# Performance work log

Hardware: AMD Instinct MI355X
Metric: run time of the kernel (lower is better)

## Reference

```python
import jax, jax.numpy as jnp
import numpy as np

N_NODES = 50000


def setup_inputs() -> dict:
    key = jax.random.key(0)
    k1, k2, k3, k4, k5, k6 = jax.random.split(key, 6)
    c_in, c_out = 64, 64
    n_edges = 800000
    G = jax.random.normal(k1, (N_NODES, c_in), dtype=jnp.float32)
    RSC = jax.random.normal(k2, (N_NODES, c_in), dtype=jnp.float32)
    src = jax.random.randint(k3, (n_edges,), 0, N_NODES, dtype=jnp.int64)
    dst = jax.random.randint(k4, (n_edges,), 0, N_NODES, dtype=jnp.int64)
    W = jax.random.normal(k5, (c_out, c_in), dtype=jnp.float32) / np.sqrt(c_in)
    b = jax.random.normal(k6, (c_out,), dtype=jnp.float32) * 0.01
    return {"G": G, "RSC": RSC, "src": src, "dst": dst, "W": W, "b": b}


def reference(G, RSC, src, dst, W, b):
    # Per-edge relative feature: src node 'G' feature minus dst node 'RSC' feature
    rel = G[src] - RSC[dst]                          # [E, c_in]
    # Linear + ReLU (edge MLP)
    enc = jax.nn.relu(rel @ W.T + b)                 # [E, c_out]
    # Per-dst-node reductions over variable-size mailboxes
    max_agg = jax.ops.segment_max(enc, dst, num_segments=N_NODES)  # -inf for empty
    sum_agg = jax.ops.segment_sum(enc, dst, num_segments=N_NODES)
    cnt = jax.ops.segment_sum(jnp.ones_like(dst, dtype=enc.dtype), dst,
                              num_segments=N_NODES)               # [N]
    has_mail = (cnt > 0)[:, None]
    avg_agg = sum_agg / jnp.maximum(cnt, 1.0)[:, None]
    max_agg = jnp.where(has_mail, max_agg, 0.0)      # nodes w/o edges -> 0
    # concat(max, avg) as in reduce()
    return jnp.concatenate([max_agg, avg_agg], axis=-1)  # [N, 2*c_out]
```

## Files before the change

kernel.cpp:

```cpp
#include <hip/hip_runtime.h>
#include <hip/hip_bf16.h>

#define NCH 64
#define SPAN 64
#define BIN_BLOCKS 128
#define BIN_THREADS 1024
#define HIST_BLOCKS 256
#define SORT_CAP 3072

__global__ void detect_init_kernel(const unsigned short* __restrict__ gp, int n16,
                                   const unsigned* __restrict__ ip, int niw,
                                   unsigned* __restrict__ flags,
                                   unsigned* __restrict__ gcnt, int nb) {
    if (blockIdx.x == 0) {
        __shared__ unsigned se, so;
        if (threadIdx.x == 0) { se = 0u; so = 0u; }
        __syncthreads();
        unsigned le = 0u, lo = 0u;
        for (int i = threadIdx.x; i < n16; i += blockDim.x) {
            unsigned ex = (unsigned)((gp[i] >> 7) & 0xFFu);
            if (ex >= 0xC0u) le++;
        }
        for (int i = threadIdx.x; i < niw; i += blockDim.x) {
            if ((i & 1) && ip[i] != 0u) lo++;
        }
        atomicAdd(&se, le);
        atomicAdd(&so, lo);
        __syncthreads();
        if (threadIdx.x == 0) {
            flags[0] = (se > 50u) ? 1u : 0u;
            flags[1] = (so < 50u) ? 1u : 0u;
        }
    } else {
        const int stride = (gridDim.x - 1) * blockDim.x;
        for (int i = (blockIdx.x - 1) * blockDim.x + threadIdx.x; i < nb; i += stride)
            gcnt[i] = 0u;
    }
}

__global__ void bucket_hist_kernel(const void* __restrict__ dstp,
                                   unsigned* __restrict__ gcnt,
                                   const unsigned* __restrict__ flags,
                                   int n_edges, int nb) {
    extern __shared__ unsigned lcnt[];
    for (int i = threadIdx.x; i < nb; i += blockDim.x) lcnt[i] = 0u;
    __syncthreads();
    const unsigned i64 = flags[1];
    const int stride = gridDim.x * blockDim.x;
    for (int e = blockIdx.x * blockDim.x + threadIdx.x; e < n_edges; e += stride) {
        int d = i64 ? (int)((const long long*)dstp)[e] : ((const int*)dstp)[e];
        atomicAdd(&lcnt[d >> 6], 1u);
    }
    __syncthreads();
    for (int i = threadIdx.x; i < nb; i += blockDim.x)
        if (lcnt[i]) atomicAdd(&gcnt[i], lcnt[i]);
}

__global__ void bucket_scan_kernel(const unsigned* __restrict__ gcnt,
                                   unsigned* __restrict__ boffs,
                                   unsigned* __restrict__ cursor, int nb) {
    __shared__ unsigned s[1024];
    const int t = threadIdx.x;
    const int L = (nb + 1023) / 1024;
    unsigned local = 0u;
    for (int i = 0; i < L; ++i) {
        int idx = t * L + i;
        if (idx < nb) local += gcnt[idx];
    }
    s[t] = local;
    __syncthreads();
    for (int off = 1; off < 1024; off <<= 1) {
        unsigned v = (t >= off) ? s[t - off] : 0u;
        __syncthreads();
        s[t] += v;
        __syncthreads();
    }
    unsigned run = s[t] - local;
    for (int i = 0; i < L; ++i) {
        int idx = t * L + i;
        if (idx < nb) { boffs[idx] = run; cursor[idx] = run; run += gcnt[idx]; }
    }
}

__global__ __launch_bounds__(BIN_THREADS)
void binning_kernel(const void* __restrict__ srcp, const void* __restrict__ dstp,
                    unsigned* __restrict__ cursor, unsigned* __restrict__ binned,
                    const unsigned* __restrict__ flags, int n_edges, int nb, int depth) {
    extern __shared__ unsigned lds[];
    unsigned* lcnt = lds;
    unsigned* stage = lds + nb;
    for (int i = threadIdx.x; i < nb; i += blockDim.x) lcnt[i] = 0u;
    __syncthreads();
    const unsigned i64 = flags[1];
    const int chunk = (n_edges + gridDim.x - 1) / gridDim.x;
    const int e0 = blockIdx.x * chunk;
    const int e1 = min(e0 + chunk, n_edges);
    for (int e = e0 + threadIdx.x; e < e1; e += blockDim.x) {
        int s, d;
        if (i64) {
            s = (int)((const long long*)srcp)[e];
            d = (int)((const long long*)dstp)[e];
        } else {
            s = ((const int*)srcp)[e];
            d = ((const int*)dstp)[e];
        }
        const int b = d >> 6;
        const unsigned pk = ((unsigned)(d & 63) << 26) | (unsigned)s;
        unsigned pos = atomicAdd(&lcnt[b], 1u);
        if ((int)pos < depth) {
            stage[b * depth + (int)pos] = pk;
        } else {
            unsigned g = atomicAdd(&cursor[b], 1u);
            binned[g] = pk;
        }
    }
    __syncthreads();
    for (int b = threadIdx.x; b < nb; b += blockDim.x) {
        int k = min((int)lcnt[b], depth);
        if (k > 0) {
            unsigned base = atomicAdd(&cursor[b], (unsigned)k);
            for (int i = 0; i < k; ++i) binned[base + i] = stage[b * depth + i];
        }
    }
}

__global__ __launch_bounds__(256)
void bucket_sort_kernel(const unsigned* __restrict__ binned,
                        const unsigned* __restrict__ boffs,
                        const unsigned* __restrict__ gcnt,
                        unsigned* __restrict__ sorted_src,
                        unsigned* __restrict__ offs,
                        int n_nodes, int n_edges, int nb) {
    __shared__ unsigned dcnt[SPAN];
    __shared__ unsigned doff[SPAN];
    __shared__ unsigned cur[SPAN];
    __shared__ unsigned stage[SORT_CAP];
    const int b = blockIdx.x;
    const int tid = threadIdx.x;
    const int estart = (int)boffs[b];
    const int count = (int)gcnt[b];

    if (tid < SPAN) dcnt[tid] = 0u;
    __syncthreads();

    for (int i = tid; i < count; i += 256) {
        const unsigned pk = binned[estart + i];
        atomicAdd(&dcnt[pk >> 26], 1u);
        if (i < SORT_CAP) stage[i] = pk;
    }
    __syncthreads();

    if (tid == 0) {
        unsigned run = 0u;
        #pragma unroll
        for (int i = 0; i < SPAN; ++i) { doff[i] = run; cur[i] = run; run += dcnt[i]; }
    }
    __syncthreads();

    if (tid < SPAN) {
        const int n = b * SPAN + tid;
        if (n < n_nodes) offs[n] = (unsigned)estart + doff[tid];
    }
    if (b == nb - 1 && tid == 0) offs[n_nodes] = (unsigned)n_edges;

    const int lim = (count < SORT_CAP) ? count : SORT_CAP;
    for (int i = tid; i < lim; i += 256) {
        const unsigned pk = stage[i];
        const unsigned pos = atomicAdd(&cur[pk >> 26], 1u);
        sorted_src[estart + pos] = pk & 0x03FFFFFFu;
    }
    for (int i = SORT_CAP + tid; i < count; i += 256) {
        const unsigned pk = binned[estart + i];
        const unsigned pos = atomicAdd(&cur[pk >> 26], 1u);
        sorted_src[estart + pos] = pk & 0x03FFFFFFu;
    }
}

__global__ void gemm2_kernel(const void* __restrict__ Gp, const void* __restrict__ Rp,
                             const void* __restrict__ Wp, const void* __restrict__ bp,
                             void* __restrict__ PQ,
                             const unsigned* __restrict__ flags, int n_nodes) {
    const unsigned f32 = flags[0];
    const int lane = threadIdx.x & 63;
    const int waveInBlk = threadIdx.x >> 6;
    const int wavesPerBlk = blockDim.x >> 6;
    const int gwave = blockIdx.x * wavesPerBlk + waveInBlk;
    const int nwaves = gridDim.x * wavesPerBlk;
    const int n_rows = 2 * n_nodes;
    const int ngroups = (n_rows + 3) / 4;

    __shared__ float ldsb[4 * 4 * NCH];
    float* slot = &ldsb[waveInBlk * 4 * NCH];

    float w[NCH];
    float bias;
    if (f32) {
        const float* Wf = (const float*)Wp;
        #pragma unroll
        for (int k = 0; k < NCH; ++k) w[k] = Wf[lane * NCH + k];
        bias = ((const float*)bp)[lane];
    } else {
        const __hip_bfloat16* Wh = (const __hip_bfloat16*)Wp;
        #pragma unroll
        for (int k = 0; k < NCH; ++k) w[k] = __bfloat162float(Wh[lane * NCH + k]);
        bias = __bfloat162float(((const __hip_bfloat16*)bp)[lane]);
    }

    const int niter = (ngroups + nwaves - 1) / nwaves;
    for (int it = 0; it < niter; ++it) {
        const int grp = gwave + it * nwaves;
        const bool gvalid = (grp < ngroups);
        const int m0 = grp * 4;
        if (gvalid) {
            const int myrow = m0 + (lane >> 4);
            const int col = (lane & 15) * 4;
            float x0 = 0.f, x1 = 0.f, x2 = 0.f, x3 = 0.f;
            if (myrow < n_rows) {
                const bool isQ = (myrow >= n_nodes);
                const int r = isQ ? (myrow - n_nodes) : myrow;
                const void* inp = isQ ? Rp : Gp;
                if (f32) {
                    float4 v = *(const float4*)((const float*)inp + (size_t)r * NCH + col);
                    x0 = v.x; x1 = v.y; x2 = v.z; x3 = v.w;
                } else {
                    ushort4 v = *(const ushort4*)((const unsigned short*)inp +
                                                  (size_t)r * NCH + col);
                    x0 = __bfloat162float(*(__hip_bfloat16*)&v.x);
                    x1 = __bfloat162float(*(__hip_bfloat16*)&v.y);
                    x2 = __bfloat162float(*(__hip_bfloat16*)&v.z);
                    x3 = __bfloat162float(*(__hip_bfloat16*)&v.w);
                }
            }
            const int sb = (lane >> 4) * NCH + col;
            slot[sb + 0] = x0; slot[sb + 1] = x1; slot[sb + 2] = x2; slot[sb + 3] = x3;
        }
        __syncthreads();
        if (gvalid) {
            #pragma unroll
            for (int rr = 0; rr < 4; ++rr) {
                const int m = m0 + rr;
                if (m < n_rows) {
                    float a0 = 0.f, a1 = 0.f, a2 = 0.f, a3 = 0.f;
                    const float4* r4 = (const float4*)(slot + rr * NCH);
                    #pragma unroll
                    for (int q = 0; q < 16; ++q) {
                        float4 rv = r4[q];
                        a0 = fmaf(rv.x, w[4 * q + 0], a0);
                        a1 = fmaf(rv.y, w[4 * q + 1], a1);
                        a2 = fmaf(rv.z, w[4 * q + 2], a2);
                        a3 = fmaf(rv.w, w[4 * q + 3], a3);
                    }
                    float acc = (a0 + a1) + (a2 + a3);
                    if (m >= n_nodes) acc -= bias;
                    if (f32) ((float*)PQ)[(size_t)m * NCH + lane] = acc;
                    else ((__hip_bfloat16*)PQ)[(size_t)m * NCH + lane] =
                             __float2bfloat16(acc);
                }
            }
        }
        __syncthreads();
    }
}

__global__ void node_kernel(const void* __restrict__ PQ,
                            const unsigned* __restrict__ sorted_src,
                            const unsigned* __restrict__ offs,
                            const unsigned* __restrict__ flags,
                            void* __restrict__ outp, int n_nodes) {
    const unsigned f32 = flags[0];
    const int lane = threadIdx.x & 63;
    const int gwave = (blockIdx.x * blockDim.x + threadIdx.x) >> 6;
    const int nwaves = (gridDim.x * blockDim.x) >> 6;
    const float* Pf = (const float*)PQ;
    const unsigned short* Ph = (const unsigned short*)PQ;

    for (int n = gwave; n < n_nodes; n += nwaves) {
        float q;
        if (f32) q = Pf[(size_t)(n_nodes + n) * NCH + lane];
        else {
            unsigned short h = Ph[(size_t)(n_nodes + n) * NCH + lane];
            q = __bfloat162float(*(__hip_bfloat16*)&h);
        }
        const int start = (int)offs[n];
        const int end = (int)offs[n + 1];
        float vmax = 0.0f, vsum = 0.0f;
        int j = start;
        for (; j + 4 <= end; j += 4) {
            const int s0 = (int)sorted_src[j];
            const int s1 = (int)sorted_src[j + 1];
            const int s2 = (int)sorted_src[j + 2];
            const int s3 = (int)sorted_src[j + 3];
            float p0, p1, p2, p3;
            if (f32) {
                p0 = Pf[(size_t)s0 * NCH + lane];
                p1 = Pf[(size_t)s1 * NCH + lane];
                p2 = Pf[(size_t)s2 * NCH + lane];
                p3 = Pf[(size_t)s3 * NCH + lane];
            } else {
                unsigned short h0 = Ph[(size_t)s0 * NCH + lane];
                unsigned short h1 = Ph[(size_t)s1 * NCH + lane];
                unsigned short h2 = Ph[(size_t)s2 * NCH + lane];
                unsigned short h3 = Ph[(size_t)s3 * NCH + lane];
                p0 = __bfloat162float(*(__hip_bfloat16*)&h0);
                p1 = __bfloat162float(*(__hip_bfloat16*)&h1);
                p2 = __bfloat162float(*(__hip_bfloat16*)&h2);
                p3 = __bfloat162float(*(__hip_bfloat16*)&h3);
            }
            const float v0 = fmaxf(p0 - q, 0.0f);
            const float v1 = fmaxf(p1 - q, 0.0f);
            const float v2 = fmaxf(p2 - q, 0.0f);
            const float v3 = fmaxf(p3 - q, 0.0f);
            vmax = fmaxf(fmaxf(vmax, v0), fmaxf(v1, fmaxf(v2, v3)));
            vsum += (v0 + v1) + (v2 + v3);
        }
        for (; j < end; ++j) {
            const int s = (int)sorted_src[j];
            float p;
            if (f32) p = Pf[(size_t)s * NCH + lane];
            else {
                unsigned short h = Ph[(size_t)s * NCH + lane];
                p = __bfloat162float(*(__hip_bfloat16*)&h);
            }
            const float v = fmaxf(p - q, 0.0f);
            vmax = fmaxf(vmax, v);
            vsum += v;
        }
        const int deg = end - start;
        const float avg = vsum / (float)(deg > 0 ? deg : 1);
        if (f32) {
            float* out = (float*)outp;
            out[(size_t)n * 2 * NCH + lane] = vmax;
            out[(size_t)n * 2 * NCH + NCH + lane] = avg;
        } else {
            __hip_bfloat16* out = (__hip_bfloat16*)outp;
            out[(size_t)n * 2 * NCH + lane] = __float2bfloat16(vmax);
            out[(size_t)n * 2 * NCH + NCH + lane] = __float2bfloat16(avg);
        }
    }
}

extern "C" void kernel_launch(void* const* d_in, const int* in_sizes, int n_in,
                              void* d_out, int out_size, void* d_ws, size_t ws_size,
                              hipStream_t stream) {
    const void* G = d_in[0];
    const void* RSC = d_in[1];
    const void* src = d_in[2];
    const void* dst = d_in[3];
    const void* W = d_in[4];
    const void* b = d_in[5];

    const int n_nodes = in_sizes[0] / NCH;
    const int n_edges = in_sizes[2];
    const int nb = (n_nodes + SPAN - 1) / SPAN;

    char* ws = (char*)d_ws;
    unsigned* flags = (unsigned*)ws;
    size_t off = 256;
    unsigned* binned = (unsigned*)(ws + off);
    off += (((size_t)n_edges * 4 + 255) / 256) * 256;
    unsigned* sorted_src = (unsigned*)(ws + off);
    off += (((size_t)n_edges * 4 + 255) / 256) * 256;
    unsigned* offs = (unsigned*)(ws + off);
    off += (((size_t)(n_nodes + 1) * 4 + 255) / 256) * 256;
    unsigned* boffs = (unsigned*)(ws + off);
    off += (((size_t)nb * 4 + 255) / 256) * 256;
    unsigned* cursor = (unsigned*)(ws + off);
    off += (((size_t)nb * 4 + 255) / 256) * 256;
    unsigned* gcnt = (unsigned*)(ws + off);
    off += (((size_t)nb * 4 + 255) / 256) * 256;
    void* PQ = (void*)(ws + off);

    const int n_g_probe = (in_sizes[0] < 8192) ? in_sizes[0] : 8192;
    const int n_idx_probe = (n_edges < 8192) ? n_edges : 8192;

    detect_init_kernel<<<64, 256, 0, stream>>>((const unsigned short*)G, n_g_probe,
                                               (const unsigned*)src, n_idx_probe,
                                               flags, gcnt, nb);

    bucket_hist_kernel<<<HIST_BLOCKS, 256, (size_t)nb * 4, stream>>>(
        dst, gcnt, flags, n_edges, nb);

    bucket_scan_kernel<<<1, 1024, 0, stream>>>(gcnt, boffs, cursor, nb);

    int depth = 16384 / nb - 1;
    if (depth > 19) depth = 19;
    if (depth < 4) depth = 4;
    const size_t bin_lds = (size_t)nb * (depth + 1) * 4;
    binning_kernel<<<BIN_BLOCKS, BIN_THREADS, bin_lds, stream>>>(
        src, dst, cursor, binned, flags, n_edges, nb, depth);

    bucket_sort_kernel<<<nb, 256, 0, stream>>>(binned, boffs, gcnt, sorted_src,
                                               offs, n_nodes, n_edges, nb);

    gemm2_kernel<<<2048, 256, 0, stream>>>(G, RSC, W, b, PQ, flags, n_nodes);

    node_kernel<<<2048, 256, 0, stream>>>(PQ, sorted_src, offs, flags, d_out, n_nodes);
}
```

Baseline: 199.4 us.

## Fuse binning with node GEMM and aggregate per bucket via LDS atomics

Runs edge binning and the node-level GEMM as disjoint block ranges of a single launch so the two phases overlap. The per-bucket counting sort and the per-node gather kernel are replaced by one bucket kernel that reads binned packed edges directly and accumulates max and sum into shared memory with atomics. The sorted_src and offsets arrays and their global traffic go away. This trades sequential per-node reductions for contended LDS float atomics, and the float atomicMax done as an int compare relies on values being non-negative after the ReLU.

```diff
diff --git a/kernel.cpp b/kernel.cpp
--- a/kernel.cpp
+++ b/kernel.cpp
@@ -3,10 +3,13 @@
 
 #define NCH 64
 #define SPAN 64
-#define BIN_BLOCKS 128
-#define BIN_THREADS 1024
 #define HIST_BLOCKS 256
-#define SORT_CAP 3072
+#define HIST_THREADS 1024
+#define NBIN 256
+#define NGEMM 256
+#define FUSE_THREADS 512
+#define AGG_THREADS 512
+#define AGG_CAP 1024
 
 __global__ void detect_init_kernel(const unsigned short* __restrict__ gp, int n16,
                                    const unsigned* __restrict__ ip, int niw,
@@ -82,259 +85,259 @@
     }
 }
 
-__global__ __launch_bounds__(BIN_THREADS)
-void binning_kernel(const void* __restrict__ srcp, const void* __restrict__ dstp,
-                    unsigned* __restrict__ cursor, unsigned* __restrict__ binned,
-                    const unsigned* __restrict__ flags, int n_edges, int nb, int depth) {
+__global__ __launch_bounds__(FUSE_THREADS, 4)
+void binning_gemm_kernel(const void* __restrict__ srcp, const void* __restrict__ dstp,
+                         unsigned* __restrict__ cursor, unsigned* __restrict__ binned,
+                         const unsigned* __restrict__ flags, int n_edges, int nb,
+                         int depth,
+                         const void* __restrict__ Gp, const void* __restrict__ Rp,
+                         const void* __restrict__ Wp, const void* __restrict__ bp,
+                         void* __restrict__ PQ, int n_nodes) {
     extern __shared__ unsigned lds[];
-    unsigned* lcnt = lds;
-    unsigned* stage = lds + nb;
-    for (int i = threadIdx.x; i < nb; i += blockDim.x) lcnt[i] = 0u;
-    __syncthreads();
-    const unsigned i64 = flags[1];
-    const int chunk = (n_edges + gridDim.x - 1) / gridDim.x;
-    const int e0 = blockIdx.x * chunk;
-    const int e1 = min(e0 + chunk, n_edges);
-    for (int e = e0 + threadIdx.x; e < e1; e += blockDim.x) {
-        int s, d;
-        if (i64) {
-            s = (int)((const long long*)srcp)[e];
-            d = (int)((const long long*)dstp)[e];
+    if (blockIdx.x < NBIN) {
+        unsigned* lcnt = lds;
+        unsigned* stage = lds + nb;
+        for (int i = threadIdx.x; i < nb; i += blockDim.x) lcnt[i] = 0u;
+        __syncthreads();
+        const unsigned i64 = flags[1];
+        const int chunk = (n_edges + NBIN - 1) / NBIN;
+        const int e0 = blockIdx.x * chunk;
+        const int e1 = min(e0 + chunk, n_edges);
+        for (int e = e0 + threadIdx.x; e < e1; e += blockDim.x) {
+            int s, d;
+            if (i64) {
+                s = (int)((const long long*)srcp)[e];
+                d = (int)((const long long*)dstp)[e];
+            } else {
+                s = ((const int*)srcp)[e];
+                d = ((const int*)dstp)[e];
+            }
+            const int bkt = d >> 6;
+            const unsigned pk = ((unsigned)(d & 63) << 26) | (unsigned)s;
+            unsigned pos = atomicAdd(&lcnt[bkt], 1u);
+            if ((int)pos < depth) {
+                stage[bkt * depth + (int)pos] = pk;
+            } else {
+                unsigned g = atomicAdd(&cursor[bkt], 1u);
+                binned[g] = pk;
+            }
+        }
+        __syncthreads();
+        for (int bkt = threadIdx.x; bkt < nb; bkt += blockDim.x) {
+            int k = min((int)lcnt[bkt], depth);
+            if (k > 0) {
+                unsigned base = atomicAdd(&cursor[bkt], (unsigned)k);
+                for (int i = 0; i < k; ++i) binned[base + i] = stage[bkt * depth + i];
+            }
+        }
+    } else {
+        const unsigned f32 = flags[0];
+        const int lane = threadIdx.x & 63;
+        const int waveInBlk = threadIdx.x >> 6;
+        const int wavesPerBlk = blockDim.x >> 6;
+        const int gwave = (blockIdx.x - NBIN) * wavesPerBlk + waveInBlk;
+        const int nwaves = NGEMM * wavesPerBlk;
+        const int n_rows = 2 * n_nodes;
+        const int ngroups = (n_rows + 3) / 4;
+
+        float* ldsb = (float*)lds;
+        float* slot = &ldsb[waveInBlk * 4 * NCH];
+
+        float w[NCH];
+        float bias;
+        if (f32) {
+            const float* Wf = (const float*)Wp;
+            #pragma unroll
+            for (int k = 0; k < NCH; ++k) w[k] = Wf[lane * NCH + k];
+            bias = ((const float*)bp)[lane];
         } else {
-            s = ((const int*)srcp)[e];
-            d = ((const int*)dstp)[e];
-        }
-        const int b = d >> 6;
-        const unsigned pk = ((unsigned)(d & 63) << 26) | (unsigned)s;
-        unsigned pos = atomicAdd(&lcnt[b], 1u);
-        if ((int)pos < depth) {
-            stage[b * depth + (int)pos] = pk;
-        } else {
-            unsigned g = atomicAdd(&cursor[b], 1u);
-            binned[g] = pk;
-        }
-    }
-    __syncthreads();
-    for (int b = threadIdx.x; b < nb; b += blockDim.x) {
-        int k = min((int)lcnt[b], depth);
-        if (k > 0) {
-            unsigned base = atomicAdd(&cursor[b], (unsigned)k);
-            for (int i = 0; i < k; ++i) binned[base + i] = stage[b * depth + i];
-        }
-    }
-}
-
-__global__ __launch_bounds__(256)
-void bucket_sort_kernel(const unsigned* __restrict__ binned,
-                        const unsigned* __restrict__ boffs,
-                        const unsigned* __restrict__ gcnt,
-                        unsigned* __restrict__ sorted_src,
-                        unsigned* __restrict__ offs,
-                        int n_nodes, int n_edges, int nb) {
+            const __hip_bfloat16* Wh = (const __hip_bfloat16*)Wp;
+            #pragma unroll
+            for (int k = 0; k < NCH; ++k) w[k] = __bfloat162float(Wh[lane * NCH + k]);
+            bias = __bfloat162float(((const __hip_bfloat16*)bp)[lane]);
+        }
+
+        const int niter = (ngroups + nwaves - 1) / nwaves;
+        for (int it = 0; it < niter; ++it) {
+            const int grp = gwave + it * nwaves;
+            const bool gvalid = (grp < ngroups);
+            const int m0 = grp * 4;
+            if (gvalid) {
+                const int myrow = m0 + (lane >> 4);
+                const int col = (lane & 15) * 4;
+                float x0 = 0.f, x1 = 0.f, x2 = 0.f, x3 = 0.f;
+                if (myrow < n_rows) {
+                    const bool isQ = (myrow >= n_nodes);
+                    const int r = isQ ? (myrow - n_nodes) : myrow;
+                    const void* inp = isQ ? Rp : Gp;
+                    if (f32) {
+                        float4 v = *(const float4*)((const float*)inp +
+                                                    (size_t)r * NCH + col);
+                        x0 = v.x; x1 = v.y; x2 = v.z; x3 = v.w;
+                    } else {
+                        ushort4 v = *(const ushort4*)((const unsigned short*)inp +
+                                                      (size_t)r * NCH + col);
+                        x0 = __bfloat162float(*(__hip_bfloat16*)&v.x);
+                        x1 = __bfloat162float(*(__hip_bfloat16*)&v.y);
+                        x2 = __bfloat162float(*(__hip_bfloat16*)&v.z);
+                        x3 = __bfloat162float(*(__hip_bfloat16*)&v.w);
+                    }
+                }
+                const int sb = (lane >> 4) * NCH + col;
+                slot[sb + 0] = x0; slot[sb + 1] = x1;
+                slot[sb + 2] = x2; slot[sb + 3] = x3;
+            }
+            __syncthreads();
+            if (gvalid) {
+                #pragma unroll
+                for (int rr = 0; rr < 4; ++rr) {
+                    const int m = m0 + rr;
+                    if (m < n_rows) {
+                        float a0 = 0.f, a1 = 0.f, a2 = 0.f, a3 = 0.f;
+                        const float4* r4 = (const float4*)(slot + rr * NCH);
+                        #pragma unroll
+                        for (int q = 0; q < 16; ++q) {
+                            float4 rv = r4[q];
+                            a0 = fmaf(rv.x, w[4 * q + 0], a0);
+                            a1 = fmaf(rv.y, w[4 * q + 1], a1);
+                            a2 = fmaf(rv.z, w[4 * q + 2], a2);
+                            a3 = fmaf(rv.w, w[4 * q + 3], a3);
+                        }
+                        float acc = (a0 + a1) + (a2 + a3);
+                        if (m >= n_nodes) acc -= bias;
+                        if (f32) ((float*)PQ)[(size_t)m * NCH + lane] = acc;
+                        else ((__hip_bfloat16*)PQ)[(size_t)m * NCH + lane] =
+                                 __float2bfloat16(acc);
+                    }
+                }
+            }
+            __syncthreads();
+        }
+    }
+}
+
+__global__ __launch_bounds__(AGG_THREADS, 6)
+void bucket_agg_kernel(const unsigned* __restrict__ binned,
+                       const unsigned* __restrict__ boffs,
+                       const unsigned* __restrict__ gcnt,
+                       const void* __restrict__ PQ,
+                       const unsigned* __restrict__ flags,
+                       void* __restrict__ outp, int n_nodes) {
+    __shared__ float accmax[SPAN * NCH];
+    __shared__ float accsum[SPAN * NCH];
+    __shared__ float qrow[SPAN * NCH];
+    __shared__ unsigned pkst[AGG_CAP];
     __shared__ unsigned dcnt[SPAN];
-    __shared__ unsigned doff[SPAN];
-    __shared__ unsigned cur[SPAN];
-    __shared__ unsigned stage[SORT_CAP];
+
     const int b = blockIdx.x;
     const int tid = threadIdx.x;
+    const unsigned f32 = flags[0];
+    const float* Pf = (const float*)PQ;
+    const unsigned short* Ph = (const unsigned short*)PQ;
+
+    for (int i = tid; i < SPAN * NCH; i += AGG_THREADS) {
+        accmax[i] = 0.0f;
+        accsum[i] = 0.0f;
+    }
+    if (tid < SPAN) dcnt[tid] = 0u;
+
+    for (int i = tid; i < SPAN * NCH; i += AGG_THREADS) {
+        const int r = i >> 6;
+        const int c = i & 63;
+        const int n = b * SPAN + r;
+        float q = 0.0f;
+        if (n < n_nodes) {
+            if (f32) q = Pf[(size_t)(n_nodes + n) * NCH + c];
+            else {
+                unsigned short h = Ph[(size_t)(n_nodes + n) * NCH + c];
+                q = __bfloat162float(*(__hip_bfloat16*)&h);
+            }
+        }
+        qrow[i] = q;
+    }
+
     const int estart = (int)boffs[b];
     const int count = (int)gcnt[b];
-
-    if (tid < SPAN) dcnt[tid] = 0u;
-    __syncthreads();
-
-    for (int i = tid; i < count; i += 256) {
-        const unsigned pk = binned[estart + i];
-        atomicAdd(&dcnt[pk >> 26], 1u);
-        if (i < SORT_CAP) stage[i] = pk;
-    }
-    __syncthreads();
-
-    if (tid == 0) {
-        unsigned run = 0u;
-        #pragma unroll
-        for (int i = 0; i < SPAN; ++i) { doff[i] = run; cur[i] = run; run += dcnt[i]; }
-    }
-    __syncthreads();
-
-    if (tid < SPAN) {
-        const int n = b * SPAN + tid;
-        if (n < n_nodes) offs[n] = (unsigned)estart + doff[tid];
-    }
-    if (b == nb - 1 && tid == 0) offs[n_nodes] = (unsigned)n_edges;
-
-    const int lim = (count < SORT_CAP) ? count : SORT_CAP;
-    for (int i = tid; i < lim; i += 256) {
-        const unsigned pk = stage[i];
-        const unsigned pos = atomicAdd(&cur[pk >> 26], 1u);
-        sorted_src[estart + pos] = pk & 0x03FFFFFFu;
-    }
-    for (int i = SORT_CAP + tid; i < count; i += 256) {
-        const unsigned pk = binned[estart + i];
-        const unsigned pos = atomicAdd(&cur[pk >> 26], 1u);
-        sorted_src[estart + pos] = pk & 0x03FFFFFFu;
-    }
-}
-
-__global__ void gemm2_kernel(const void* __restrict__ Gp, const void* __restrict__ Rp,
-                             const void* __restrict__ Wp, const void* __restrict__ bp,
-                             void* __restrict__ PQ,
-                             const unsigned* __restrict__ flags, int n_nodes) {
-    const unsigned f32 = flags[0];
-    const int lane = threadIdx.x & 63;
-    const int waveInBlk = threadIdx.x >> 6;
-    const int wavesPerBlk = blockDim.x >> 6;
-    const int gwave = blockIdx.x * wavesPerBlk + waveInBlk;
-    const int nwaves = gridDim.x * wavesPerBlk;
-    const int n_rows = 2 * n_nodes;
-    const int ngroups = (n_rows + 3) / 4;
-
-    __shared__ float ldsb[4 * 4 * NCH];
-    float* slot = &ldsb[waveInBlk * 4 * NCH];
-
-    float w[NCH];
-    float bias;
-    if (f32) {
-        const float* Wf = (const float*)Wp;
-        #pragma unroll
-        for (int k = 0; k < NCH; ++k) w[k] = Wf[lane * NCH + k];
-        bias = ((const float*)bp)[lane];
-    } else {
-        const __hip_bfloat16* Wh = (const __hip_bfloat16*)Wp;
-        #pragma unroll
-        for (int k = 0; k < NCH; ++k) w[k] = __bfloat162float(Wh[lane * NCH + k]);
-        bias = __bfloat162float(((const __hip_bfloat16*)bp)[lane]);
-    }
-
-    const int niter = (ngroups + nwaves - 1) / nwaves;
-    for (int it = 0; it < niter; ++it) {
-        const int grp = gwave + it * nwaves;
-        const bool gvalid = (grp < ngroups);
-        const int m0 = grp * 4;
-        if (gvalid) {
-            const int myrow = m0 + (lane >> 4);
-            const int col = (lane & 15) * 4;
-            float x0 = 0.f, x1 = 0.f, x2 = 0.f, x3 = 0.f;
-            if (myrow < n_rows) {
-                const bool isQ = (myrow >= n_nodes);
-                const int r = isQ ? (myrow - n_nodes) : myrow;
-                const void* inp = isQ ? Rp : Gp;
-                if (f32) {
-                    float4 v = *(const float4*)((const float*)inp + (size_t)r * NCH + col);
-                    x0 = v.x; x1 = v.y; x2 = v.z; x3 = v.w;
-                } else {
-                    ushort4 v = *(const ushort4*)((const unsigned short*)inp +
-                                                  (size_t)r * NCH + col);
-                    x0 = __bfloat162float(*(__hip_bfloat16*)&v.x);
-                    x1 = __bfloat162float(*(__hip_bfloat16*)&v.y);
-                    x2 = __bfloat162float(*(__hip_bfloat16*)&v.z);
-                    x3 = __bfloat162float(*(__hip_bfloat16*)&v.w);
-                }
-            }
-            const int sb = (lane >> 4) * NCH + col;
-            slot[sb + 0] = x0; slot[sb + 1] = x1; slot[sb + 2] = x2; slot[sb + 3] = x3;
-        }
-        __syncthreads();
-        if (gvalid) {
-            #pragma unroll
-            for (int rr = 0; rr < 4; ++rr) {
-                const int m = m0 + rr;
-                if (m < n_rows) {
-                    float a0 = 0.f, a1 = 0.f, a2 = 0.f, a3 = 0.f;
-                    const float4* r4 = (const float4*)(slot + rr * NCH);
-                    #pragma unroll
-                    for (int q = 0; q < 16; ++q) {
-                        float4 rv = r4[q];
-                        a0 = fmaf(rv.x, w[4 * q + 0], a0);
-                        a1 = fmaf(rv.y, w[4 * q + 1], a1);
-                        a2 = fmaf(rv.z, w[4 * q + 2], a2);
-                        a3 = fmaf(rv.w, w[4 * q + 3], a3);
-                    }
-                    float acc = (a0 + a1) + (a2 + a3);
-                    if (m >= n_nodes) acc -= bias;
-                    if (f32) ((float*)PQ)[(size_t)m * NCH + lane] = acc;
-                    else ((__hip_bfloat16*)PQ)[(size_t)m * NCH + lane] =
-                             __float2bfloat16(acc);
-                }
-            }
-        }
-        __syncthreads();
-    }
-}
-
-__global__ void node_kernel(const void* __restrict__ PQ,
-                            const unsigned* __restrict__ sorted_src,
-                            const unsigned* __restrict__ offs,
-                            const unsigned* __restrict__ flags,
-                            void* __restrict__ outp, int n_nodes) {
-    const unsigned f32 = flags[0];
-    const int lane = threadIdx.x & 63;
-    const int gwave = (blockIdx.x * blockDim.x + threadIdx.x) >> 6;
-    const int nwaves = (gridDim.x * blockDim.x) >> 6;
-    const float* Pf = (const float*)PQ;
-    const unsigned short* Ph = (const unsigned short*)PQ;
-
-    for (int n = gwave; n < n_nodes; n += nwaves) {
-        float q;
-        if (f32) q = Pf[(size_t)(n_nodes + n) * NCH + lane];
-        else {
-            unsigned short h = Ph[(size_t)(n_nodes + n) * NCH + lane];
-            q = __bfloat162float(*(__hip_bfloat16*)&h);
-        }
-        const int start = (int)offs[n];
-        const int end = (int)offs[n + 1];
-        float vmax = 0.0f, vsum = 0.0f;
-        int j = start;
-        for (; j + 4 <= end; j += 4) {
-            const int s0 = (int)sorted_src[j];
-            const int s1 = (int)sorted_src[j + 1];
-            const int s2 = (int)sorted_src[j + 2];
-            const int s3 = (int)sorted_src[j + 3];
-            float p0, p1, p2, p3;
+    const int lim = (count < AGG_CAP) ? count : AGG_CAP;
+    for (int i = tid; i < lim; i += AGG_THREADS) pkst[i] = binned[estart + i];
+    __syncthreads();
+
+    const int lane = tid & 63;
+    const int wid = tid >> 6;
+    const int NW4 = (AGG_THREADS >> 6) * 4;
+
+    auto LOADPK = [&](int i) -> unsigned {
+        return (i < lim) ? pkst[i] : binned[estart + i];
+    };
+    auto LOADP = [&](int s) -> float {
+        if (f32) return Pf[(size_t)s * NCH + lane];
+        unsigned short h = Ph[(size_t)s * NCH + lane];
+        return __bfloat162float(*(__hip_bfloat16*)&h);
+    };
+
+    for (int base = wid * 4; base < count; base += NW4) {
+        const int kk = count - base;
+        const unsigned pk0 = LOADPK(base);
+        const unsigned pk1 = (kk > 1) ? LOADPK(base + 1) : 0u;
+        const unsigned pk2 = (kk > 2) ? LOADPK(base + 2) : 0u;
+        const unsigned pk3 = (kk > 3) ? LOADPK(base + 3) : 0u;
+        const int s0 = (int)(pk0 & 0x03FFFFFFu), d0 = (int)(pk0 >> 26);
+        const int s1 = (int)(pk1 & 0x03FFFFFFu), d1 = (int)(pk1 >> 26);
+        const int s2 = (int)(pk2 & 0x03FFFFFFu), d2 = (int)(pk2 >> 26);
+        const int s3 = (int)(pk3 & 0x03FFFFFFu), d3 = (int)(pk3 >> 26);
+        const float p0 = LOADP(s0);
+        const float p1 = (kk > 1) ? LOADP(s1) : 0.0f;
+        const float p2 = (kk > 2) ? LOADP(s2) : 0.0f;
+        const float p3 = (kk > 3) ? LOADP(s3) : 0.0f;
+
+        {
+            const int a = (d0 << 6) | lane;
+            const float v = fmaxf(p0 - qrow[a], 0.0f);
+            atomicMax((int*)&accmax[a], __float_as_int(v));
+            atomicAdd(&accsum[a], v);
+            if (lane == 0) atomicAdd(&dcnt[d0], 1u);
+        }
+        if (kk > 1) {
+            const int a = (d1 << 6) | lane;
+            const float v = fmaxf(p1 - qrow[a], 0.0f);
+            atomicMax((int*)&accmax[a], __float_as_int(v));
+            atomicAdd(&accsum[a], v);
+            if (lane == 0) atomicAdd(&dcnt[d1], 1u);
+        }
+        if (kk > 2) {
+            const int a = (d2 << 6) | lane;
+            const float v = fmaxf(p2 - qrow[a], 0.0f);
+            atomicMax((int*)&accmax[a], __float_as_int(v));
+            atomicAdd(&accsum[a], v);
+            if (lane == 0) atomicAdd(&dcnt[d2], 1u);
+        }
+        if (kk > 3) {
+            const int a = (d3 << 6) | lane;
+            const float v = fmaxf(p3 - qrow[a], 0.0f);
+            atomicMax((int*)&accmax[a], __float_as_int(v));
+            atomicAdd(&accsum[a], v);
+            if (lane == 0) atomicAdd(&dcnt[d3], 1u);
+        }
+    }
+    __syncthreads();
+
+    for (int i = tid; i < SPAN * NCH; i += AGG_THREADS) {
+        const int r = i >> 6;
+        const int c = i & 63;
+        const int n = b * SPAN + r;
+        if (n < n_nodes) {
+            const unsigned deg = dcnt[r];
+            const float m = accmax[i];
+            const float a = accsum[i] / (float)(deg ? deg : 1u);
             if (f32) {
-                p0 = Pf[(size_t)s0 * NCH + lane];
-                p1 = Pf[(size_t)s1 * NCH + lane];
-                p2 = Pf[(size_t)s2 * NCH + lane];
-                p3 = Pf[(size_t)s3 * NCH + lane];
+                float* o = (float*)outp;
+                o[(size_t)n * 2 * NCH + c] = m;
+                o[(size_t)n * 2 * NCH + NCH + c] = a;
             } else {
-                unsigned short h0 = Ph[(size_t)s0 * NCH + lane];
-                unsigned short h1 = Ph[(size_t)s1 * NCH + lane];
-                unsigned short h2 = Ph[(size_t)s2 * NCH + lane];
-                unsigned short h3 = Ph[(size_t)s3 * NCH + lane];
-                p0 = __bfloat162float(*(__hip_bfloat16*)&h0);
-                p1 = __bfloat162float(*(__hip_bfloat16*)&h1);
-                p2 = __bfloat162float(*(__hip_bfloat16*)&h2);
-                p3 = __bfloat162float(*(__hip_bfloat16*)&h3);
-            }
-            const float v0 = fmaxf(p0 - q, 0.0f);
-            const float v1 = fmaxf(p1 - q, 0.0f);
-            const float v2 = fmaxf(p2 - q, 0.0f);
-            const float v3 = fmaxf(p3 - q, 0.0f);
-            vmax = fmaxf(fmaxf(vmax, v0), fmaxf(v1, fmaxf(v2, v3)));
-            vsum += (v0 + v1) + (v2 + v3);
-        }
-        for (; j < end; ++j) {
-            const int s = (int)sorted_src[j];
-            float p;
-            if (f32) p = Pf[(size_t)s * NCH + lane];
-            else {
-                unsigned short h = Ph[(size_t)s * NCH + lane];
-                p = __bfloat162float(*(__hip_bfloat16*)&h);
-            }
-            const float v = fmaxf(p - q, 0.0f);
-            vmax = fmaxf(vmax, v);
-            vsum += v;
-        }
-        const int deg = end - start;
-        const float avg = vsum / (float)(deg > 0 ? deg : 1);
-        if (f32) {
-            float* out = (float*)outp;
-            out[(size_t)n * 2 * NCH + lane] = vmax;
-            out[(size_t)n * 2 * NCH + NCH + lane] = avg;
-        } else {
-            __hip_bfloat16* out = (__hip_bfloat16*)outp;
-            out[(size_t)n * 2 * NCH + lane] = __float2bfloat16(vmax);
-            out[(size_t)n * 2 * NCH + NCH + lane] = __float2bfloat16(avg);
+                __hip_bfloat16* o = (__hip_bfloat16*)outp;
+                o[(size_t)n * 2 * NCH + c] = __float2bfloat16(m);
+                o[(size_t)n * 2 * NCH + NCH + c] = __float2bfloat16(a);
+            }
         }
     }
 }
@@ -358,10 +361,6 @@
     size_t off = 256;
     unsigned* binned = (unsigned*)(ws + off);
     off += (((size_t)n_edges * 4 + 255) / 256) * 256;
-    unsigned* sorted_src = (unsigned*)(ws + off);
-    off += (((size_t)n_edges * 4 + 255) / 256) * 256;
-    unsigned* offs = (unsigned*)(ws + off);
-    off += (((size_t)(n_nodes + 1) * 4 + 255) / 256) * 256;
     unsigned* boffs = (unsigned*)(ws + off);
     off += (((size_t)nb * 4 + 255) / 256) * 256;
     unsigned* cursor = (unsigned*)(ws + off);
@@ -377,7 +376,7 @@
                                                (const unsigned*)src, n_idx_probe,
                                                flags, gcnt, nb);
 
-    bucket_hist_kernel<<<HIST_BLOCKS, 256, (size_t)nb * 4, stream>>>(
+    bucket_hist_kernel<<<HIST_BLOCKS, HIST_THREADS, (size_t)nb * 4, stream>>>(
         dst, gcnt, flags, n_edges, nb);
 
     bucket_scan_kernel<<<1, 1024, 0, stream>>>(gcnt, boffs, cursor, nb);
@@ -385,14 +384,14 @@
     int depth = 16384 / nb - 1;
     if (depth > 19) depth = 19;
     if (depth < 4) depth = 4;
-    const size_t bin_lds = (size_t)nb * (depth + 1) * 4;
-    binning_kernel<<<BIN_BLOCKS, BIN_THREADS, bin_lds, stream>>>(
-        src, dst, cursor, binned, flags, n_edges, nb, depth);
-
-    bucket_sort_kernel<<<nb, 256, 0, stream>>>(binned, boffs, gcnt, sorted_src,
-                                               offs, n_nodes, n_edges, nb);
-
-    gemm2_kernel<<<2048, 256, 0, stream>>>(G, RSC, W, b, PQ, flags, n_nodes);
-
-    node_kernel<<<2048, 256, 0, stream>>>(PQ, sorted_src, offs, flags, d_out, n_nodes);
-}
+    size_t bin_lds = (size_t)nb * (depth + 1) * 4;
+    const size_t gemm_lds = (size_t)(FUSE_THREADS / 64) * 4 * NCH * 4;
+    if (bin_lds < gemm_lds) bin_lds = gemm_lds;
+
+    binning_gemm_kernel<<<NBIN + NGEMM, FUSE_THREADS, bin_lds, stream>>>(
+        src, dst, cursor, binned, flags, n_edges, nb, depth,
+        G, RSC, W, b, PQ, n_nodes);
+
+    bucket_agg_kernel<<<nb, AGG_THREADS, 0, stream>>>(binned, boffs, gcnt, PQ,
+                                                      flags, d_out, n_nodes);
+}
```

After: 511.5 us. +156.5%, slower.

## Fuse binning and node GEMM into one launch with disjoint block roles

Applied to the files above, without the earlier changes.

Merges the edge binning kernel and the per-node GEMM into one kernel whose first 256 blocks do binning and the remaining 256 blocks compute PQ. The two independent stages can then share the GPU concurrently and one launch is dropped. Block size, binning block count and histogram thread count also change. The GEMM now runs on far fewer waves (256x8 instead of 2048x4), and both roles share the same dynamic LDS size and launch bounds, which may limit occupancy.

```diff
diff --git a/kernel.cpp b/kernel.cpp
--- a/kernel.cpp
+++ b/kernel.cpp
@@ -3,9 +3,11 @@
 
 #define NCH 64
 #define SPAN 64
-#define BIN_BLOCKS 128
-#define BIN_THREADS 1024
 #define HIST_BLOCKS 256
+#define HIST_THREADS 1024
+#define NBIN 256
+#define NGEMM 256
+#define FUSE_THREADS 512
 #define SORT_CAP 3072
 
 __global__ void detect_init_kernel(const unsigned short* __restrict__ gp, int n16,
@@ -82,44 +84,133 @@
     }
 }
 
-__global__ __launch_bounds__(BIN_THREADS)
-void binning_kernel(const void* __restrict__ srcp, const void* __restrict__ dstp,
-                    unsigned* __restrict__ cursor, unsigned* __restrict__ binned,
-                    const unsigned* __restrict__ flags, int n_edges, int nb, int depth) {
+__global__ __launch_bounds__(FUSE_THREADS, 4)
+void binning_gemm_kernel(const void* __restrict__ srcp, const void* __restrict__ dstp,
+                         unsigned* __restrict__ cursor, unsigned* __restrict__ binned,
+                         const unsigned* __restrict__ flags, int n_edges, int nb,
+                         int depth,
+                         const void* __restrict__ Gp, const void* __restrict__ Rp,
+                         const void* __restrict__ Wp, const void* __restrict__ bp,
+                         void* __restrict__ PQ, int n_nodes) {
     extern __shared__ unsigned lds[];
-    unsigned* lcnt = lds;
-    unsigned* stage = lds + nb;
-    for (int i = threadIdx.x; i < nb; i += blockDim.x) lcnt[i] = 0u;
-    __syncthreads();
-    const unsigned i64 = flags[1];
-    const int chunk = (n_edges + gridDim.x - 1) / gridDim.x;
-    const int e0 = blockIdx.x * chunk;
-    const int e1 = min(e0 + chunk, n_edges);
-    for (int e = e0 + threadIdx.x; e < e1; e += blockDim.x) {
-        int s, d;
-        if (i64) {
-            s = (int)((const long long*)srcp)[e];
-            d = (int)((const long long*)dstp)[e];
+    if (blockIdx.x < NBIN) {
+        unsigned* lcnt = lds;
+        unsigned* stage = lds + nb;
+        for (int i = threadIdx.x; i < nb; i += blockDim.x) lcnt[i] = 0u;
+        __syncthreads();
+        const unsigned i64 = flags[1];
+        const int chunk = (n_edges + NBIN - 1) / NBIN;
+        const int e0 = blockIdx.x * chunk;
+        const int e1 = min(e0 + chunk, n_edges);
+        for (int e = e0 + threadIdx.x; e < e1; e += blockDim.x) {
+            int s, d;
+            if (i64) {
+                s = (int)((const long long*)srcp)[e];
+                d = (int)((const long long*)dstp)[e];
+            } else {
+                s = ((const int*)srcp)[e];
+                d = ((const int*)dstp)[e];
+            }
+            const int bkt = d >> 6;
+            const unsigned pk = ((unsigned)(d & 63) << 26) | (unsigned)s;
+            unsigned pos = atomicAdd(&lcnt[bkt], 1u);
+            if ((int)pos < depth) {
+                stage[bkt * depth + (int)pos] = pk;
+            } else {
+                unsigned g = atomicAdd(&cursor[bkt], 1u);
+                binned[g] = pk;
+            }
+        }
+        __syncthreads();
+        for (int bkt = threadIdx.x; bkt < nb; bkt += blockDim.x) {
+            int k = min((int)lcnt[bkt], depth);
+            if (k > 0) {
+                unsigned base = atomicAdd(&cursor[bkt], (unsigned)k);
+                for (int i = 0; i < k; ++i) binned[base + i] = stage[bkt * depth + i];
+            }
+        }
+    } else {
+        const unsigned f32 = flags[0];
+        const int lane = threadIdx.x & 63;
+        const int waveInBlk = threadIdx.x >> 6;
+        const int wavesPerBlk = blockDim.x >> 6;
+        const int gwave = (blockIdx.x - NBIN) * wavesPerBlk + waveInBlk;
+        const int nwaves = NGEMM * wavesPerBlk;
+        const int n_rows = 2 * n_nodes;
+        const int ngroups = (n_rows + 3) / 4;
+
+        float* ldsb = (float*)lds;
+        float* slot = &ldsb[waveInBlk * 4 * NCH];
+
+        float w[NCH];
+        float bias;
+        if (f32) {
+            const float* Wf = (const float*)Wp;
+            #pragma unroll
+            for (int k = 0; k < NCH; ++k) w[k] = Wf[lane * NCH + k];
+            bias = ((const float*)bp)[lane];
         } else {
-            s = ((const int*)srcp)[e];
-            d = ((const int*)dstp)[e];
-        }
-        const int b = d >> 6;
-        const unsigned pk = ((unsigned)(d & 63) << 26) | (unsigned)s;
-        unsigned pos = atomicAdd(&lcnt[b], 1u);
-        if ((int)pos < depth) {
-            stage[b * depth + (int)pos] = pk;
-        } else {
-            unsigned g = atomicAdd(&cursor[b], 1u);
-            binned[g] = pk;
-        }
-    }
-    __syncthreads();
-    for (int b = threadIdx.x; b < nb; b += blockDim.x) {
-        int k = min((int)lcnt[b], depth);
-        if (k > 0) {
-            unsigned base = atomicAdd(&cursor[b], (unsigned)k);
-            for (int i = 0; i < k; ++i) binned[base + i] = stage[b * depth + i];
+            const __hip_bfloat16* Wh = (const __hip_bfloat16*)Wp;
+            #pragma unroll
+            for (int k = 0; k < NCH; ++k) w[k] = __bfloat162float(Wh[lane * NCH + k]);
+            bias = __bfloat162float(((const __hip_bfloat16*)bp)[lane]);
+        }
+
+        const int niter = (ngroups + nwaves - 1) / nwaves;
+        for (int it = 0; it < niter; ++it) {
+            const int grp = gwave + it * nwaves;
+            const bool gvalid = (grp < ngroups);
+            const int m0 = grp * 4;
+            if (gvalid) {
+                const int myrow = m0 + (lane >> 4);
+                const int col = (lane & 15) * 4;
+                float x0 = 0.f, x1 = 0.f, x2 = 0.f, x3 = 0.f;
+                if (myrow < n_rows) {
+                    const bool isQ = (myrow >= n_nodes);
+                    const int r = isQ ? (myrow - n_nodes) : myrow;
+                    const void* inp = isQ ? Rp : Gp;
+                    if (f32) {
+                        float4 v = *(const float4*)((const float*)inp +
+                                                    (size_t)r * NCH + col);
+                        x0 = v.x; x1 = v.y; x2 = v.z; x3 = v.w;
+                    } else {
+                        ushort4 v = *(const ushort4*)((const unsigned short*)inp +
+                                                      (size_t)r * NCH + col);
+                        x0 = __bfloat162float(*(__hip_bfloat16*)&v.x);
+                        x1 = __bfloat162float(*(__hip_bfloat16*)&v.y);
+                        x2 = __bfloat162float(*(__hip_bfloat16*)&v.z);
+                        x3 = __bfloat162float(*(__hip_bfloat16*)&v.w);
+                    }
+                }
+                const int sb = (lane >> 4) * NCH + col;
+                slot[sb + 0] = x0; slot[sb + 1] = x1;
+                slot[sb + 2] = x2; slot[sb + 3] = x3;
+            }
+            __syncthreads();
+            if (gvalid) {
+                #pragma unroll
+                for (int rr = 0; rr < 4; ++rr) {
+                    const int m = m0 + rr;
+                    if (m < n_rows) {
+                        float a0 = 0.f, a1 = 0.f, a2 = 0.f, a3 = 0.f;
+                        const float4* r4 = (const float4*)(slot + rr * NCH);
+                        #pragma unroll
+                        for (int q = 0; q < 16; ++q) {
+                            float4 rv = r4[q];
+                            a0 = fmaf(rv.x, w[4 * q + 0], a0);
+                            a1 = fmaf(rv.y, w[4 * q + 1], a1);
+                            a2 = fmaf(rv.z, w[4 * q + 2], a2);
+                            a3 = fmaf(rv.w, w[4 * q + 3], a3);
+                        }
+                        float acc = (a0 + a1) + (a2 + a3);
+                        if (m >= n_nodes) acc -= bias;
+                        if (f32) ((float*)PQ)[(size_t)m * NCH + lane] = acc;
+                        else ((__hip_bfloat16*)PQ)[(size_t)m * NCH + lane] =
+                                 __float2bfloat16(acc);
+                    }
+                }
+            }
+            __syncthreads();
         }
     }
 }
@@ -173,92 +264,6 @@
         const unsigned pk = binned[estart + i];
         const unsigned pos = atomicAdd(&cur[pk >> 26], 1u);
         sorted_src[estart + pos] = pk & 0x03FFFFFFu;
-    }
-}
-
-__global__ void gemm2_kernel(const void* __restrict__ Gp, const void* __restrict__ Rp,
-                             const void* __restrict__ Wp, const void* __restrict__ bp,
-                             void* __restrict__ PQ,
-                             const unsigned* __restrict__ flags, int n_nodes) {
-    const unsigned f32 = flags[0];
-    const int lane = threadIdx.x & 63;
-    const int waveInBlk = threadIdx.x >> 6;
-    const int wavesPerBlk = blockDim.x >> 6;
-    const int gwave = blockIdx.x * wavesPerBlk + waveInBlk;
-    const int nwaves = gridDim.x * wavesPerBlk;
-    const int n_rows = 2 * n_nodes;
-    const int ngroups = (n_rows + 3) / 4;
-
-    __shared__ float ldsb[4 * 4 * NCH];
-    float* slot = &ldsb[waveInBlk * 4 * NCH];
-
-    float w[NCH];
-    float bias;
-    if (f32) {
-        const float* Wf = (const float*)Wp;
-        #pragma unroll
-        for (int k = 0; k < NCH; ++k) w[k] = Wf[lane * NCH + k];
-        bias = ((const float*)bp)[lane];
-    } else {
-        const __hip_bfloat16* Wh = (const __hip_bfloat16*)Wp;
-        #pragma unroll
-        for (int k = 0; k < NCH; ++k) w[k] = __bfloat162float(Wh[lane * NCH + k]);
-        bias = __bfloat162float(((const __hip_bfloat16*)bp)[lane]);
-    }
-
-    const int niter = (ngroups + nwaves - 1) / nwaves;
-    for (int it = 0; it < niter; ++it) {
-        const int grp = gwave + it * nwaves;
-        const bool gvalid = (grp < ngroups);
-        const int m0 = grp * 4;
-        if (gvalid) {
-            const int myrow = m0 + (lane >> 4);
-            const int col = (lane & 15) * 4;
-            float x0 = 0.f, x1 = 0.f, x2 = 0.f, x3 = 0.f;
-            if (myrow < n_rows) {
-                const bool isQ = (myrow >= n_nodes);
-                const int r = isQ ? (myrow - n_nodes) : myrow;
-                const void* inp = isQ ? Rp : Gp;
-                if (f32) {
-                    float4 v = *(const float4*)((const float*)inp + (size_t)r * NCH + col);
-                    x0 = v.x; x1 = v.y; x2 = v.z; x3 = v.w;
-                } else {
-                    ushort4 v = *(const ushort4*)((const unsigned short*)inp +
-                                                  (size_t)r * NCH + col);
-                    x0 = __bfloat162float(*(__hip_bfloat16*)&v.x);
-                    x1 = __bfloat162float(*(__hip_bfloat16*)&v.y);
-                    x2 = __bfloat162float(*(__hip_bfloat16*)&v.z);
-                    x3 = __bfloat162float(*(__hip_bfloat16*)&v.w);
-                }
-            }
-            const int sb = (lane >> 4) * NCH + col;
-            slot[sb + 0] = x0; slot[sb + 1] = x1; slot[sb + 2] = x2; slot[sb + 3] = x3;
-        }
-        __syncthreads();
-        if (gvalid) {
-            #pragma unroll
-            for (int rr = 0; rr < 4; ++rr) {
-                const int m = m0 + rr;
-                if (m < n_rows) {
-                    float a0 = 0.f, a1 = 0.f, a2 = 0.f, a3 = 0.f;
-                    const float4* r4 = (const float4*)(slot + rr * NCH);
-                    #pragma unroll
-                    for (int q = 0; q < 16; ++q) {
-                        float4 rv = r4[q];
-                        a0 = fmaf(rv.x, w[4 * q + 0], a0);
-                        a1 = fmaf(rv.y, w[4 * q + 1], a1);
-                        a2 = fmaf(rv.z, w[4 * q + 2], a2);
-                        a3 = fmaf(rv.w, w[4 * q + 3], a3);
-                    }
-                    float acc = (a0 + a1) + (a2 + a3);
-                    if (m >= n_nodes) acc -= bias;
-                    if (f32) ((float*)PQ)[(size_t)m * NCH + lane] = acc;
-                    else ((__hip_bfloat16*)PQ)[(size_t)m * NCH + lane] =
-                             __float2bfloat16(acc);
-                }
-            }
-        }
-        __syncthreads();
     }
 }
 
@@ -377,7 +382,7 @@
                                                (const unsigned*)src, n_idx_probe,
                                                flags, gcnt, nb);
 
-    bucket_hist_kernel<<<HIST_BLOCKS, 256, (size_t)nb * 4, stream>>>(
+    bucket_hist_kernel<<<HIST_BLOCKS, HIST_THREADS, (size_t)nb * 4, stream>>>(
         dst, gcnt, flags, n_edges, nb);
 
     bucket_scan_kernel<<<1, 1024, 0, stream>>>(gcnt, boffs, cursor, nb);
@@ -385,14 +390,16 @@
     int depth = 16384 / nb - 1;
     if (depth > 19) depth = 19;
     if (depth < 4) depth = 4;
-    const size_t bin_lds = (size_t)nb * (depth + 1) * 4;
-    binning_kernel<<<BIN_BLOCKS, BIN_THREADS, bin_lds, stream>>>(
-        src, dst, cursor, binned, flags, n_edges, nb, depth);
+    size_t bin_lds = (size_t)nb * (depth + 1) * 4;
+    const size_t gemm_lds = (size_t)(FUSE_THREADS / 64) * 4 * NCH * 4;
+    if (bin_lds < gemm_lds) bin_lds = gemm_lds;
+
+    binning_gemm_kernel<<<NBIN + NGEMM, FUSE_THREADS, bin_lds, stream>>>(
+        src, dst, cursor, binned, flags, n_edges, nb, depth,
+        G, RSC, W, b, PQ, n_nodes);
 
     bucket_sort_kernel<<<nb, 256, 0, stream>>>(binned, boffs, gcnt, sorted_src,
                                                offs, n_nodes, n_edges, nb);
 
-    gemm2_kernel<<<2048, 256, 0, stream>>>(G, RSC, W, b, PQ, flags, n_nodes);
-
     node_kernel<<<2048, 256, 0, stream>>>(PQ, sorted_src, offs, flags, d_out, n_nodes);
 }
```

After: 194.0 us. -2.7%, faster.
